# Optimization experiments

Measured on AMD Instinct MI355X. Metric: run time of the kernel, lower is better.

Reference implementation:

```python
import math
import jax, jax.numpy as jnp
import numpy as np

D_MODEL = 1024
N_HEADS = 16
D_K = D_MODEL // N_HEADS
THETA = 10000.0
B, S = 2, 2048


def setup_inputs() -> dict:
    key = jax.random.key(0)
    k1, k2, k3 = jax.random.split(key, 3)
    x = jax.random.normal(k1, (B, S, D_MODEL), dtype=jnp.float32)
    token_positions = jnp.arange(B * S, dtype=jnp.int32).reshape(B, S)
    std_qkv = math.sqrt(2.0 / (D_MODEL + 3 * D_MODEL))
    std_o = math.sqrt(2.0 / (D_MODEL + D_MODEL))
    W_qkv = jax.random.truncated_normal(k2, -3.0, 3.0, (3 * D_MODEL, D_MODEL), dtype=jnp.float32) * std_qkv
    W_o = jax.random.truncated_normal(k3, -3.0, 3.0, (D_MODEL, D_MODEL), dtype=jnp.float32) * std_o
    return {"x": x, "W_qkv": W_qkv, "W_o": W_o, "token_positions": token_positions}


def _rope(x, pos):
    # x: (B, H, S, D_K); pos: (B, S) int
    half = D_K // 2
    inv_freq = 1.0 / (THETA ** (jnp.arange(0, D_K, 2, dtype=jnp.float32) / D_K))  # (half,)
    # pos_extended = pos[:, None, :] -> freqs (B, 1, S, half)
    freqs = pos[:, None, :, None].astype(jnp.float32) * inv_freq
    cos, sin = jnp.cos(freqs), jnp.sin(freqs)
    xr = x.reshape(*x.shape[:-1], half, 2)
    x1, x2 = xr[..., 0], xr[..., 1]
    out = jnp.stack([x1 * cos - x2 * sin, x2 * cos + x1 * sin], axis=-1)
    return out.reshape(x.shape)


def reference(x, W_qkv, W_o, token_positions):
    seq_len = x.shape[-2]
    qkv = jnp.einsum('bsi,oi->bso', x, W_qkv)
    q, k, v = jnp.split(qkv, 3, axis=-1)
    # (B, S, H*D) -> (B, H, S, D)
    def to_heads(t):
        return t.reshape(t.shape[0], t.shape[1], N_HEADS, D_K).transpose(0, 2, 1, 3)
    q, k, v = to_heads(q), to_heads(k), to_heads(v)
    q = _rope(q, token_positions)
    k = _rope(k, token_positions)
    scores = jnp.einsum('bhnd,bhmd->bhnm', q, k) / math.sqrt(D_K)
    causal = jnp.tril(jnp.ones((seq_len, seq_len), dtype=bool))
    scores = jnp.where(causal, scores, -jnp.inf)
    attn = jax.nn.softmax(scores, axis=-1)
    out = jnp.einsum('bhnm,bhmd->bhnd', attn, v)
    out = out.transpose(0, 2, 1, 3).reshape(x.shape[0], seq_len, D_MODEL)
    return jnp.einsum('bsi,oi->bso', out, W_o)
```

## Files before the change

kernel.cpp:

```cpp
#include <hip/hip_runtime.h>
#include <cmath>

typedef __bf16 bf16;
typedef bf16 bf16x4 __attribute__((ext_vector_type(4)));
typedef bf16 bf16x8 __attribute__((ext_vector_type(8)));
typedef float f32x4 __attribute__((ext_vector_type(4)));

#define MFMA16(a, b, c) __builtin_amdgcn_mfma_f32_16x16x32_bf16(a, b, c, 0, 0, 0)

#define GLOAD16(g, l)                                                   \
  __builtin_amdgcn_global_load_lds(                                     \
      (const __attribute__((address_space(1))) unsigned int*)(g),       \
      (__attribute__((address_space(3))) unsigned int*)(l), 16, 0, 0)

__global__ __launch_bounds__(256) void cvt_all(
    const float* __restrict__ x, const float* __restrict__ wqkv,
    const float* __restrict__ wo, bf16* __restrict__ xb,
    bf16* __restrict__ wqkvb, bf16* __restrict__ wob) {
  int i = (blockIdx.x * 256 + threadIdx.x) * 4;
  const float* src;
  bf16* dst;
  if (i < (4 << 20)) {
    src = x + i; dst = xb + i;
  } else if (i < (7 << 20)) {
    src = wqkv + (i - (4 << 20)); dst = wqkvb + (i - (4 << 20));
  } else {
    src = wo + (i - (7 << 20)); dst = wob + (i - (7 << 20));
  }
  const f32x4 v = *(const f32x4*)src;
  bf16x4 o = {(bf16)v[0], (bf16)v[1], (bf16)v[2], (bf16)v[3]};
  *(bf16x4*)dst = o;
}

template <int EPI, int BN>
__global__ __launch_bounds__(256) void gemm_nt(
    const bf16* __restrict__ A, const bf16* __restrict__ Bm,
    const int* __restrict__ tokpos,
    bf16* __restrict__ out0, bf16* __restrict__ out1, bf16* __restrict__ out2,
    float* __restrict__ outF, int N) {
  constexpr int NI = BN / 32;
  constexpr int TSTRIDE = 136;
  __shared__ __align__(16) union SMem {
    struct { bf16 A[2][128 * 32]; bf16 B[2][BN * 32]; } st;
    bf16 T[EPI ? 128 * TSTRIDE : 1];
  } sm;
  const int tid = threadIdx.x;
  const int w = tid >> 6, lane = tid & 63, quad = lane >> 4, m16 = lane & 15;
  const int m0 = blockIdx.y * 128, n0 = blockIdx.x * BN;
  const int wm = (w >> 1) * 64, wn = (w & 1) * (BN / 2);

  f32x4 acc[4][NI] = {};

  const int row0 = tid >> 2, ch = tid & 3;
  const bf16* Ag0 = A + (size_t)(m0 + row0) * 1024 + ch * 8;
  const bf16* Ag1 = Ag0 + (size_t)64 * 1024;
  const bf16* Bg0 = Bm + (size_t)(n0 + row0) * 1024 + ch * 8;
  const bf16* Bg1 = Bg0 + (size_t)64 * 1024;

  auto STAGE = [&](int p, int k0) {
    GLOAD16(Ag0 + k0, &sm.st.A[p][tid * 8]);
    GLOAD16(Ag1 + k0, &sm.st.A[p][2048 + tid * 8]);
    GLOAD16(Bg0 + k0, &sm.st.B[p][tid * 8]);
    if constexpr (BN == 128) GLOAD16(Bg1 + k0, &sm.st.B[p][2048 + tid * 8]);
  };

  STAGE(0, 0);
  __syncthreads();

  int p = 0;
  for (int k0 = 0; k0 < 1024; k0 += 32) {
    const bool more = (k0 + 32) < 1024;
    if (more) STAGE(p ^ 1, k0 + 32);
    bf16x8 af[4], bfr[NI];
#pragma unroll
    for (int mi = 0; mi < 4; ++mi)
      af[mi] =
          *(const bf16x8*)(&sm.st.A[p][(wm + mi * 16 + m16) * 32 + quad * 8]);
#pragma unroll
    for (int ni = 0; ni < NI; ++ni)
      bfr[ni] =
          *(const bf16x8*)(&sm.st.B[p][(wn + ni * 16 + m16) * 32 + quad * 8]);
#pragma unroll
    for (int mi = 0; mi < 4; ++mi)
#pragma unroll
      for (int ni = 0; ni < NI; ++ni)
        acc[mi][ni] = MFMA16(af[mi], bfr[ni], acc[mi][ni]);
    if (more) {
      __syncthreads();
      p ^= 1;
    }
  }

  if constexpr (EPI == 0) {
#pragma unroll
    for (int mi = 0; mi < 4; ++mi) {
      int rowb = m0 + wm + mi * 16 + quad * 4;
#pragma unroll
      for (int r = 0; r < 4; ++r) {
        size_t off = (size_t)(rowb + r) * N + n0 + wn;
#pragma unroll
        for (int ni = 0; ni < NI; ++ni)
          outF[off + ni * 16 + m16] = acc[mi][ni][r];
      }
    }
  } else {
    const int secb = n0 >> 10;
    if (secb == 2) {
      __syncthreads();
#pragma unroll
      for (int mi = 0; mi < 4; ++mi) {
        int rlb = wm + mi * 16 + quad * 4;
#pragma unroll
        for (int ni = 0; ni < 4; ++ni) {
          int c = wn + ni * 16 + m16;
          bf16x4 pk = {(bf16)acc[mi][ni][0], (bf16)acc[mi][ni][1],
                       (bf16)acc[mi][ni][2], (bf16)acc[mi][ni][3]};
          *(bf16x4*)(&sm.T[c * TSTRIDE + rlb]) = pk;
        }
      }
      __syncthreads();
      const int bb = m0 >> 11, S0 = m0 & 2047;
      const size_t base = ((size_t)bb * 1024 + (n0 - 2048)) * 2048 + S0;
#pragma unroll
      for (int it = 0; it < 8; ++it) {
        int chunk = it * 256 + tid;
        int c = chunk >> 4, kp = (chunk & 15) * 8;
        bf16x8 v = *(const bf16x8*)(&sm.T[c * TSTRIDE + kp]);
        *(bf16x8*)(out2 + base + (size_t)c * 2048 + kp) = v;
      }
    } else {
      bf16* dst = secb ? out1 : out0;
      const float sc = secb ? 1.0f : 0.125f;
#pragma unroll
      for (int mi = 0; mi < 4; ++mi) {
        int rowb = m0 + wm + mi * 16 + quad * 4;
        int pos4[4];
#pragma unroll
        for (int r = 0; r < 4; ++r) pos4[r] = tokpos[rowb + r];
#pragma unroll
        for (int ni = 0; ni < 4; ++ni) {
          int col = n0 + wn + ni * 16 + m16;
          int f = col & 1023, h = f >> 6, d = f & 63;
          float inv = __expf(-(float)(d & ~1) * (9.2103403719762f / 64.f));
#pragma unroll
          for (int r = 0; r < 4; ++r) {
            float v = acc[mi][ni][r];
            float vp = __shfl_xor(v, 1);
            float ang = (float)pos4[r] * inv;
            float cs, sn;
            __sincosf(ang, &sn, &cs);
            float ov = (d & 1) ? (v * cs + vp * sn) : (v * cs - vp * sn);
            ov *= sc;
            int row = rowb + r;
            int bb = row >> 11, s = row & 2047;
            dst[((size_t)(bb * 16 + h) * 2048 + s) * 64 + d] = (bf16)ov;
          }
        }
      }
    }
  }
}

__global__ __launch_bounds__(256) void attn_kernel(
    const bf16* __restrict__ Q, const bf16* __restrict__ K,
    const bf16* __restrict__ Vt, bf16* __restrict__ O) {
  __shared__ __align__(16) bf16 KP[3][64 * 72];
  __shared__ __align__(16) bf16 VP[3][64 * 72];
  __shared__ __align__(16) bf16 PS[4][16 * 72];
  const int tid = threadIdx.x;
  const int w = tid >> 6, lane = tid & 63, quad = lane >> 4, m16 = lane & 15;
  const int bh = blockIdx.x;
  const int j = blockIdx.y;
  const int qtA = j, qtB = 31 - j;
  const int q0A = qtA * 64, q0B = qtB * 64;
  const bf16* Qb = Q + (size_t)bh * 2048 * 64;
  const bf16* Kb = K + (size_t)bh * 2048 * 64;
  const bf16* Vb = Vt + (size_t)bh * 64 * 2048;

  const int ch0 = w * 8, ch1 = (w + 4) * 8;
  const bf16* Kg = Kb + (size_t)lane * 64;
  const bf16* Vg = Vb + (size_t)lane * 2048;

  const bf16* qrowA = Qb + (size_t)(q0A + w * 16 + m16) * 64;
  const bf16* qrowB = Qb + (size_t)(q0B + w * 16 + m16) * 64;
  bf16x8 aqA[2], aqB[2];
  aqA[0] = *(const bf16x8*)(qrowA + quad * 8);
  aqA[1] = *(const bf16x8*)(qrowA + 32 + quad * 8);
  aqB[0] = *(const bf16x8*)(qrowB + quad * 8);
  aqB[1] = *(const bf16x8*)(qrowB + 32 + quad * 8);

  bf16x8 rk0, rk1, rv0, rv1;
  auto PREFETCH = [&](int kt) {
    rk0 = *(const bf16x8*)(Kg + (size_t)kt * 64 * 64 + ch0);
    rk1 = *(const bf16x8*)(Kg + (size_t)kt * 64 * 64 + ch1);
    rv0 = *(const bf16x8*)(Vg + kt * 64 + ch0);
    rv1 = *(const bf16x8*)(Vg + kt * 64 + ch1);
  };
  auto STAGE = [&](int p) {
    *(bf16x8*)(KP[p] + lane * 72 + ch0) = rk0;
    *(bf16x8*)(KP[p] + lane * 72 + ch1) = rk1;
    *(bf16x8*)(VP[p] + lane * 72 + ch0) = rv0;
    *(bf16x8*)(VP[p] + lane * 72 + ch1) = rv1;
  };

  PREFETCH(0);
  STAGE(0);
  PREFETCH(1);
  STAGE(1);
  __syncthreads();

  auto QK = [&](int p, const bf16x8* aq, f32x4* sa) {
    __builtin_amdgcn_s_setprio(1);
#pragma unroll
    for (int kk = 0; kk < 2; ++kk)
#pragma unroll
      for (int ni = 0; ni < 4; ++ni) {
        bf16x8 bk = *(const bf16x8*)(KP[p] + (ni * 16 + m16) * 72 + kk * 32 +
                                     quad * 8);
        sa[ni] = MFMA16(aq[kk], bk, sa[ni]);
      }
    __builtin_amdgcn_s_setprio(0);
  };

  f32x4 oA[4] = {}, oB[4] = {};
  float lA[4] = {0.f, 0.f, 0.f, 0.f}, lB[4] = {0.f, 0.f, 0.f, 0.f};
  const int qrel = w * 16 + quad * 4;

  auto SOFTPV = [&](int p, const f32x4* sa, f32x4* o, float* lp, bool diag) {
    bf16* ps = PS[w];
#pragma unroll
    for (int r = 0; r < 4; ++r) {
#pragma unroll
      for (int ni = 0; ni < 4; ++ni) {
        float pp = exp2f(fmaf(sa[ni][r], 1.44269504f, -11.5415603f));
        if (diag && (ni * 16 + m16) > qrel + r) pp = 0.f;
        lp[r] += pp;
        ps[(quad * 4 + r) * 72 + ni * 16 + m16] = (bf16)pp;
      }
    }
    bf16x8 ap[2];
    ap[0] = *(const bf16x8*)(ps + m16 * 72 + quad * 8);
    ap[1] = *(const bf16x8*)(ps + m16 * 72 + 32 + quad * 8);
    __builtin_amdgcn_s_setprio(1);
#pragma unroll
    for (int kk = 0; kk < 2; ++kk)
#pragma unroll
      for (int ng = 0; ng < 4; ++ng) {
        bf16x8 bv = *(const bf16x8*)(VP[p] + (ng * 16 + m16) * 72 + kk * 32 +
                                     quad * 8);
        o[ng] = MFMA16(ap[kk], bv, o[ng]);
      }
    __builtin_amdgcn_s_setprio(0);
  };

  f32x4 saA[4] = {}, saB[4] = {};
  QK(0, aqB, saB);
  QK(0, aqA, saA);

  int pc = 0, pn = 1, pst = 2;
  for (int kt = 0; kt <= qtB; ++kt) {
    const bool more = kt < qtB;
    const bool stage2 = (kt + 2) <= qtB;
    if (stage2) PREFETCH(kt + 2);

    f32x4 saBn[4] = {}, saAn[4] = {};
    if (more) QK(pn, aqB, saBn);
    if (kt + 1 <= qtA) QK(pn, aqA, saAn);

    SOFTPV(pc, saB, oB, lB, kt == qtB);
    if (kt <= qtA) SOFTPV(pc, saA, oA, lA, kt == qtA);

    if (stage2) STAGE(pst);
    if (more) __syncthreads();

#pragma unroll
    for (int i = 0; i < 4; ++i) { saB[i] = saBn[i]; saA[i] = saAn[i]; }
    int t = pc; pc = pn; pn = pst; pst = t;
  }

  const int b = bh >> 4, h = bh & 15;
  auto epilogue = [&](f32x4* o, float* lp, int q0) {
#pragma unroll
    for (int r = 0; r < 4; ++r) {
      float l = lp[r];
      l += __shfl_xor(l, 1);
      l += __shfl_xor(l, 2);
      l += __shfl_xor(l, 4);
      l += __shfl_xor(l, 8);
      float inv_l = 1.f / l;
      int s = q0 + w * 16 + quad * 4 + r;
      size_t rowoff = (size_t)(b * 2048 + s) * 1024 + h * 64;
#pragma unroll
      for (int ng = 0; ng < 4; ++ng)
        O[rowoff + ng * 16 + m16] = (bf16)(o[ng][r] * inv_l);
    }
  };
  epilogue(oA, lA, q0A);
  epilogue(oB, lB, q0B);
}

extern "C" void kernel_launch(void* const* d_in, const int* in_sizes, int n_in,
                              void* d_out, int out_size, void* d_ws, size_t ws_size,
                              hipStream_t stream) {
  (void)in_sizes; (void)n_in; (void)out_size; (void)ws_size;
  const float* x = (const float*)d_in[0];
  const float* Wqkv = (const float*)d_in[1];
  const float* Wo = (const float*)d_in[2];
  const int* tokpos = (const int*)d_in[3];
  float* out = (float*)d_out;

  const size_t NEL = (size_t)2 * 16 * 2048 * 64;
  bf16* Qws = (bf16*)d_ws;
  bf16* Kws = Qws + NEL;
  bf16* Vtw = Kws + NEL;
  bf16* Ows = Vtw + NEL;
  bf16* xb  = Ows + NEL;
  bf16* Wqkvb = xb + NEL;
  bf16* Wob = Wqkvb + (size_t)3072 * 1024;

  cvt_all<<<8192, 256, 0, stream>>>(x, Wqkv, Wo, xb, Wqkvb, Wob);

  gemm_nt<1, 128><<<dim3(24, 32), 256, 0, stream>>>(xb, Wqkvb, tokpos, Qws,
                                                    Kws, Vtw, nullptr, 3072);
  attn_kernel<<<dim3(32, 16), 256, 0, stream>>>(Qws, Kws, Vtw, Ows);
  gemm_nt<0, 64><<<dim3(16, 32), 256, 0, stream>>>(Ows, Wob, nullptr, nullptr,
                                                   nullptr, nullptr, out, 1024);
}
```

Measured before the change: 187.5 us.

## Restructure attention to one query tile per block with direct-to-LDS swizzled loads

Each attention block now handles a single 64-row query tile instead of a paired (j, 31-j) tile pair, and the grid is doubled with heavy tiles launched first. K/V tiles are loaded straight into LDS with global_load_lds instead of passing through registers, into an XOR-swizzled unpadded layout that is double-buffered rather than triple-buffered. The cross-iteration software pipelining of QK against softmax/PV is removed, which simplifies the code and cuts register and LDS use, at the cost of load balance within a block and less overlap between matrix ops.

```diff
diff --git a/kernel.cpp b/kernel.cpp
--- a/kernel.cpp
+++ b/kernel.cpp
@@ -164,139 +164,110 @@
 __global__ __launch_bounds__(256) void attn_kernel(
     const bf16* __restrict__ Q, const bf16* __restrict__ K,
     const bf16* __restrict__ Vt, bf16* __restrict__ O) {
-  __shared__ __align__(16) bf16 KP[3][64 * 72];
-  __shared__ __align__(16) bf16 VP[3][64 * 72];
-  __shared__ __align__(16) bf16 PS[4][16 * 72];
+  __shared__ __align__(16) bf16 KP[2][64 * 64];
+  __shared__ __align__(16) bf16 VP[2][64 * 64];
+  __shared__ __align__(16) bf16 PS[4][16 * 64];
   const int tid = threadIdx.x;
   const int w = tid >> 6, lane = tid & 63, quad = lane >> 4, m16 = lane & 15;
+  const int h8 = m16 >> 3, ml = m16 & 7;
   const int bh = blockIdx.x;
-  const int j = blockIdx.y;
-  const int qtA = j, qtB = 31 - j;
-  const int q0A = qtA * 64, q0B = qtB * 64;
+  const int j = 31 - blockIdx.y;
   const bf16* Qb = Q + (size_t)bh * 2048 * 64;
   const bf16* Kb = K + (size_t)bh * 2048 * 64;
   const bf16* Vb = Vt + (size_t)bh * 64 * 2048;
 
-  const int ch0 = w * 8, ch1 = (w + 4) * 8;
-  const bf16* Kg = Kb + (size_t)lane * 64;
-  const bf16* Vg = Vb + (size_t)lane * 2048;
-
-  const bf16* qrowA = Qb + (size_t)(q0A + w * 16 + m16) * 64;
-  const bf16* qrowB = Qb + (size_t)(q0B + w * 16 + m16) * 64;
-  bf16x8 aqA[2], aqB[2];
-  aqA[0] = *(const bf16x8*)(qrowA + quad * 8);
-  aqA[1] = *(const bf16x8*)(qrowA + 32 + quad * 8);
-  aqB[0] = *(const bf16x8*)(qrowB + quad * 8);
-  aqB[1] = *(const bf16x8*)(qrowB + 32 + quad * 8);
-
-  bf16x8 rk0, rk1, rv0, rv1;
-  auto PREFETCH = [&](int kt) {
-    rk0 = *(const bf16x8*)(Kg + (size_t)kt * 64 * 64 + ch0);
-    rk1 = *(const bf16x8*)(Kg + (size_t)kt * 64 * 64 + ch1);
-    rv0 = *(const bf16x8*)(Vg + kt * 64 + ch0);
-    rv1 = *(const bf16x8*)(Vg + kt * 64 + ch1);
+  const int srow = tid >> 3, sc = (tid & 7) ^ (srow & 7);
+  const bf16* Kg = Kb + (size_t)srow * 64 + sc * 8;
+  const bf16* Vg = Vb + (size_t)srow * 2048 + sc * 8;
+  auto GSTAGE = [&](int kt, int p) {
+    const bf16* kg = Kg + (size_t)kt * 4096;
+    const bf16* vg = Vg + kt * 64;
+    GLOAD16(kg, &KP[p][tid * 8]);
+    GLOAD16(kg + (size_t)32 * 64, &KP[p][2048 + tid * 8]);
+    GLOAD16(vg, &VP[p][tid * 8]);
+    GLOAD16(vg + (size_t)32 * 2048, &VP[p][2048 + tid * 8]);
   };
-  auto STAGE = [&](int p) {
-    *(bf16x8*)(KP[p] + lane * 72 + ch0) = rk0;
-    *(bf16x8*)(KP[p] + lane * 72 + ch1) = rk1;
-    *(bf16x8*)(VP[p] + lane * 72 + ch0) = rv0;
-    *(bf16x8*)(VP[p] + lane * 72 + ch1) = rv1;
-  };
-
-  PREFETCH(0);
-  STAGE(0);
-  PREFETCH(1);
-  STAGE(1);
+
+  const bf16* qrow = Qb + (size_t)(j * 64 + w * 16 + m16) * 64;
+  bf16x8 aq[2];
+  aq[0] = *(const bf16x8*)(qrow + quad * 8);
+  aq[1] = *(const bf16x8*)(qrow + 32 + quad * 8);
+
+  GSTAGE(0, 0);
   __syncthreads();
 
-  auto QK = [&](int p, const bf16x8* aq, f32x4* sa) {
+  f32x4 o[4] = {};
+  float l4[4] = {0.f, 0.f, 0.f, 0.f};
+  const int qrel = w * 16 + quad * 4;
+  bf16* ps = PS[w];
+
+  int p = 0;
+  for (int kt = 0; kt <= j; ++kt) {
+    const bool more = kt < j;
+    if (more) GSTAGE(kt + 1, p ^ 1);
+
+    f32x4 sa[4] = {};
     __builtin_amdgcn_s_setprio(1);
 #pragma unroll
     for (int kk = 0; kk < 2; ++kk)
 #pragma unroll
       for (int ni = 0; ni < 4; ++ni) {
-        bf16x8 bk = *(const bf16x8*)(KP[p] + (ni * 16 + m16) * 72 + kk * 32 +
-                                     quad * 8);
+        bf16x8 bk = *(const bf16x8*)(
+            &KP[p][(ni * 16 + m16) * 64 + (((kk * 4 + quad) ^ ml) << 3)]);
         sa[ni] = MFMA16(aq[kk], bk, sa[ni]);
       }
     __builtin_amdgcn_s_setprio(0);
-  };
-
-  f32x4 oA[4] = {}, oB[4] = {};
-  float lA[4] = {0.f, 0.f, 0.f, 0.f}, lB[4] = {0.f, 0.f, 0.f, 0.f};
-  const int qrel = w * 16 + quad * 4;
-
-  auto SOFTPV = [&](int p, const f32x4* sa, f32x4* o, float* lp, bool diag) {
-    bf16* ps = PS[w];
+
+    const bool diag = (kt == j);
 #pragma unroll
     for (int r = 0; r < 4; ++r) {
+      const int prow = quad * 4 + r;
+      const int rb = prow * 64, rx = prow & 7;
 #pragma unroll
       for (int ni = 0; ni < 4; ++ni) {
         float pp = exp2f(fmaf(sa[ni][r], 1.44269504f, -11.5415603f));
         if (diag && (ni * 16 + m16) > qrel + r) pp = 0.f;
-        lp[r] += pp;
-        ps[(quad * 4 + r) * 72 + ni * 16 + m16] = (bf16)pp;
+        l4[r] += pp;
+        ps[rb + (((ni * 2 + h8) ^ rx) << 3) + ml] = (bf16)pp;
       }
     }
     bf16x8 ap[2];
-    ap[0] = *(const bf16x8*)(ps + m16 * 72 + quad * 8);
-    ap[1] = *(const bf16x8*)(ps + m16 * 72 + 32 + quad * 8);
+#pragma unroll
+    for (int kk = 0; kk < 2; ++kk)
+      ap[kk] =
+          *(const bf16x8*)(&ps[m16 * 64 + (((kk * 4 + quad) ^ ml) << 3)]);
     __builtin_amdgcn_s_setprio(1);
 #pragma unroll
     for (int kk = 0; kk < 2; ++kk)
 #pragma unroll
       for (int ng = 0; ng < 4; ++ng) {
-        bf16x8 bv = *(const bf16x8*)(VP[p] + (ng * 16 + m16) * 72 + kk * 32 +
-                                     quad * 8);
+        bf16x8 bv = *(const bf16x8*)(
+            &VP[p][(ng * 16 + m16) * 64 + (((kk * 4 + quad) ^ ml) << 3)]);
         o[ng] = MFMA16(ap[kk], bv, o[ng]);
       }
     __builtin_amdgcn_s_setprio(0);
-  };
-
-  f32x4 saA[4] = {}, saB[4] = {};
-  QK(0, aqB, saB);
-  QK(0, aqA, saA);
-
-  int pc = 0, pn = 1, pst = 2;
-  for (int kt = 0; kt <= qtB; ++kt) {
-    const bool more = kt < qtB;
-    const bool stage2 = (kt + 2) <= qtB;
-    if (stage2) PREFETCH(kt + 2);
-
-    f32x4 saBn[4] = {}, saAn[4] = {};
-    if (more) QK(pn, aqB, saBn);
-    if (kt + 1 <= qtA) QK(pn, aqA, saAn);
-
-    SOFTPV(pc, saB, oB, lB, kt == qtB);
-    if (kt <= qtA) SOFTPV(pc, saA, oA, lA, kt == qtA);
-
-    if (stage2) STAGE(pst);
-    if (more) __syncthreads();
-
-#pragma unroll
-    for (int i = 0; i < 4; ++i) { saB[i] = saBn[i]; saA[i] = saAn[i]; }
-    int t = pc; pc = pn; pn = pst; pst = t;
-  }
-
-  const int b = bh >> 4, h = bh & 15;
-  auto epilogue = [&](f32x4* o, float* lp, int q0) {
-#pragma unroll
-    for (int r = 0; r < 4; ++r) {
-      float l = lp[r];
-      l += __shfl_xor(l, 1);
-      l += __shfl_xor(l, 2);
-      l += __shfl_xor(l, 4);
-      l += __shfl_xor(l, 8);
-      float inv_l = 1.f / l;
-      int s = q0 + w * 16 + quad * 4 + r;
-      size_t rowoff = (size_t)(b * 2048 + s) * 1024 + h * 64;
-#pragma unroll
-      for (int ng = 0; ng < 4; ++ng)
-        O[rowoff + ng * 16 + m16] = (bf16)(o[ng][r] * inv_l);
-    }
-  };
-  epilogue(oA, lA, q0A);
-  epilogue(oB, lB, q0B);
+
+    if (more) {
+      __syncthreads();
+      p ^= 1;
+    }
+  }
+
+  const int b = bh >> 4, hh = bh & 15;
+#pragma unroll
+  for (int r = 0; r < 4; ++r) {
+    float l = l4[r];
+    l += __shfl_xor(l, 1);
+    l += __shfl_xor(l, 2);
+    l += __shfl_xor(l, 4);
+    l += __shfl_xor(l, 8);
+    float inv_l = 1.f / l;
+    int s = j * 64 + w * 16 + quad * 4 + r;
+    size_t rowoff = (size_t)(b * 2048 + s) * 1024 + hh * 64;
+#pragma unroll
+    for (int ng = 0; ng < 4; ++ng)
+      O[rowoff + ng * 16 + m16] = (bf16)(o[ng][r] * inv_l);
+  }
 }
 
 extern "C" void kernel_launch(void* const* d_in, const int* in_sizes, int n_in,
@@ -322,7 +293,7 @@
 
   gemm_nt<1, 128><<<dim3(24, 32), 256, 0, stream>>>(xb, Wqkvb, tokpos, Qws,
                                                     Kws, Vtw, nullptr, 3072);
-  attn_kernel<<<dim3(32, 16), 256, 0, stream>>>(Qws, Kws, Vtw, Ows);
+  attn_kernel<<<dim3(32, 32), 256, 0, stream>>>(Qws, Kws, Vtw, Ows);
   gemm_nt<0, 64><<<dim3(16, 32), 256, 0, stream>>>(Ows, Wob, nullptr, nullptr,
                                                    nullptr, nullptr, out, 1024);
 }
```

After: 180.5 us. 1.04x faster.
